# Kernel optimization log

Hardware: AMD Instinct MI355X
Metric: run time of the kernel (lower is better)

## Reference

```python
import jax, jax.numpy as jnp
import numpy as np

BS, SEQ, DIN, HID, H = 2, 2048, 1024, 1024, 16
D = HID // H  # head_size = 64

def setup_inputs() -> dict:
    key = jax.random.key(0)
    ks = jax.random.split(key, 9)
    s = 0.02
    return {
        "x":    jax.random.normal(ks[0], (BS, SEQ, DIN), jnp.float32),
        "Wq":   jax.random.normal(ks[1], (DIN, HID), jnp.float32) * s,
        "bq":   jax.random.normal(ks[2], (HID,), jnp.float32) * s,
        "Wk":   jax.random.normal(ks[3], (DIN, HID), jnp.float32) * s,
        "bk":   jax.random.normal(ks[4], (HID,), jnp.float32) * s,
        "Wv":   jax.random.normal(ks[5], (DIN, HID), jnp.float32) * s,
        "bv":   jax.random.normal(ks[6], (HID,), jnp.float32) * s,
        "Wmix": jax.random.normal(ks[7], (HID, HID), jnp.float32) * s,
        "bmix": jax.random.normal(ks[8], (HID,), jnp.float32) * s,
    }

def reference(x, Wq, bq, Wk, bk, Wv, bv, Wmix, bmix):
    bs, seq, _ = x.shape
    scale = jnp.asarray(D ** 0.5, x.dtype)
    # projections, split heads: [b, s, H, D] (contiguous channel slices per head,
    # equivalent to the torch transpose/reshape dance)
    q = (x @ Wq + bq).reshape(bs, seq, H, D)
    k = (x @ Wk + bk).reshape(bs, seq, H, D)
    v = (x @ Wv + bv).reshape(bs, seq, H, D)
    scores = jnp.einsum('bqhd,bkhd->bhqk', q, k) / scale  # [b, H, seq, seq]
    causal_mask = jnp.triu(jnp.ones((seq, seq), bool), k=1)
    scores = jnp.where(causal_mask, -jnp.inf, scores)
    probs = jax.nn.softmax(scores, axis=-1)
    att = jnp.einsum('bhqk,bkhd->bqhd', probs, v).reshape(bs, seq, HID)
    return att @ Wmix + bmix
```

## Files before the change

### kernel.cpp

```cpp
#include <hip/hip_runtime.h>
#include <hip/hip_bf16.h>

#define BS 2
#define SEQ 2048
#define DIN 1024
#define HID 1024
#define NH 16
#define HD 64
#define M_ROWS (BS*SEQ)
#define NQKV 3072

typedef __attribute__((ext_vector_type(8))) short short8;
typedef __attribute__((ext_vector_type(4))) short short4v;
typedef __attribute__((ext_vector_type(8))) __bf16 bf16x8;
typedef __attribute__((ext_vector_type(4))) float floatx4;

__device__ __forceinline__ short f2bf(float f) {
  return __builtin_bit_cast(short, (__bf16)f);
}
__device__ __forceinline__ float bf2f(short s) {
  return __uint_as_float(((unsigned)(unsigned short)s) << 16);
}

__device__ __forceinline__ floatx4 mfma16(short8 a, short8 b, floatx4 c) {
  return __builtin_amdgcn_mfma_f32_16x16x32_bf16(
      __builtin_bit_cast(bf16x8, a), __builtin_bit_cast(bf16x8, b), c, 0, 0, 0);
}

__device__ __forceinline__ float exp2fast(float x) {
#if __has_builtin(__builtin_amdgcn_exp2f)
  return __builtin_amdgcn_exp2f(x);
#else
  return exp2f(x);
#endif
}

__device__ __forceinline__ void gload_lds16(const void* g, void* l) {
  __builtin_amdgcn_global_load_lds(
      (const __attribute__((address_space(1))) unsigned int*)g,
      (__attribute__((address_space(3))) unsigned int*)l, 16, 0, 0);
}

__device__ __forceinline__ void lds_w8s(short* base, int row, int colsh, short8 v) {
  *(short8*)((char*)base + row * 128 + ((colsh * 2) ^ ((row & 7) << 4))) = v;
}
__device__ __forceinline__ void lds_w4s(short* base, int row, int colsh, short4v v) {
  *(short4v*)((char*)base + row * 128 + ((colsh * 2) ^ ((row & 7) << 4))) = v;
}
__device__ __forceinline__ short8 lds_r8s(const short* base, int row, int colsh) {
  return *(const short8*)((const char*)base + row * 128 + ((colsh * 2) ^ ((row & 7) << 4)));
}

__global__ __launch_bounds__(256) void convx_kernel(const float* __restrict__ x,
                                                    short* __restrict__ xb) {
  int gid = blockIdx.x * 256 + threadIdx.x;
  const float4* x4 = (const float4*)x;
  float4 v0 = x4[2 * gid], v1 = x4[2 * gid + 1];
  short8 o;
  o[0] = f2bf(v0.x); o[1] = f2bf(v0.y); o[2] = f2bf(v0.z); o[3] = f2bf(v0.w);
  o[4] = f2bf(v1.x); o[5] = f2bf(v1.y); o[6] = f2bf(v1.z); o[7] = f2bf(v1.w);
  *(short8*)&xb[(size_t)gid * 8] = o;
}

__global__ __launch_bounds__(256) void transw_kernel(
    const float* __restrict__ Wq, const float* __restrict__ Wk,
    const float* __restrict__ Wv, const float* __restrict__ Wmix,
    short* __restrict__ Wt, short* __restrict__ Wmixt)
{
  __shared__ float Ws[64][65];
  const float* src; short* dst;
  switch (blockIdx.z) {
    case 0:  src = Wq;   dst = Wt;                 break;
    case 1:  src = Wk;   dst = Wt + (1u << 20);    break;
    case 2:  src = Wv;   dst = Wt + (2u << 20);    break;
    default: src = Wmix; dst = Wmixt;              break;
  }
  const int n0 = blockIdx.x * 64, k0 = blockIdx.y * 64;
  const int c = threadIdx.x & 63, r0 = threadIdx.x >> 6;
  #pragma unroll
  for (int i = 0; i < 16; ++i) {
    int rr = r0 + 4 * i;
    Ws[rr][c] = src[(size_t)(k0 + rr) * DIN + n0 + c];
  }
  __syncthreads();
  #pragma unroll
  for (int i = 0; i < 16; ++i) {
    int cc = r0 + 4 * i;
    dst[(size_t)(n0 + cc) * DIN + k0 + c] = f2bf(Ws[c][cc]);
  }
}

template<int BM, int BN, bool OUT_F32, bool QKV>
__global__ __launch_bounds__(256) void gemm_kernel(
    const short* __restrict__ A, const short* __restrict__ Bt,
    const float* __restrict__ bias0, const float* __restrict__ bias1,
    const float* __restrict__ bias2, void* __restrict__ Cp,
    short* __restrict__ vt, int Ndim, int Kdim)
{
  constexpr int MT = BM / 32, NT = BN / 32;
  __shared__ short As[BM * 64];
  __shared__ short Bs[BN * 64];
  const int tid = threadIdx.x;
  const int wid = tid >> 6, lane = tid & 63, lg = lane >> 4, lm = lane & 15;
  const int wr = wid >> 1, wc = wid & 1;
  const int m0 = blockIdx.y * BM, n0 = blockIdx.x * BN;

  floatx4 acc[MT][NT];
  #pragma unroll
  for (int i = 0; i < MT; ++i)
    #pragma unroll
    for (int j = 0; j < NT; ++j) acc[i][j] = floatx4{0.f, 0.f, 0.f, 0.f};

  for (int k0 = 0; k0 < Kdim; k0 += 64) {
    __syncthreads();
    #pragma unroll
    for (int j = 0; j < BM / 32; ++j) {
      int flat = tid + 256 * j;
      int row = flat >> 3, ch = (flat & 7) ^ (row & 7);
      gload_lds16(A + (size_t)(m0 + row) * Kdim + k0 + ch * 8,
                  (char*)As + wid * 1024 + j * 4096);
    }
    #pragma unroll
    for (int j = 0; j < BN / 32; ++j) {
      int flat = tid + 256 * j;
      int row = flat >> 3, ch = (flat & 7) ^ (row & 7);
      gload_lds16(Bt + (size_t)(n0 + row) * Kdim + k0 + ch * 8,
                  (char*)Bs + wid * 1024 + j * 4096);
    }
    __syncthreads();

    #pragma unroll
    for (int kk = 0; kk < 2; ++kk) {
      short8 a[MT], b[NT];
      #pragma unroll
      for (int mt = 0; mt < MT; ++mt) {
        int row = wr * (BM / 2) + mt * 16 + lm;
        int ch = (kk * 4 + lg) ^ (row & 7);
        a[mt] = *(const short8*)&As[row * 64 + ch * 8];
      }
      #pragma unroll
      for (int nt = 0; nt < NT; ++nt) {
        int row = wc * (BN / 2) + nt * 16 + lm;
        int ch = (kk * 4 + lg) ^ (row & 7);
        b[nt] = *(const short8*)&Bs[row * 64 + ch * 8];
      }
      #pragma unroll
      for (int mt = 0; mt < MT; ++mt)
        #pragma unroll
        for (int nt = 0; nt < NT; ++nt)
          acc[mt][nt] = mfma16(a[mt], b[nt], acc[mt][nt]);
    }
  }

  #pragma unroll
  for (int mt = 0; mt < MT; ++mt) {
    const int row0 = m0 + wr * (BM / 2) + mt * 16 + 4 * lg;
    #pragma unroll
    for (int nt = 0; nt < NT; ++nt) {
      const int col = n0 + wc * (BN / 2) + nt * 16 + lm;
      const float* bp = bias0;
      if (QKV) bp = (col < 1024) ? bias0 : (col < 2048 ? bias1 : bias2);
      const float bv = bp[col & 1023];
      if (QKV && n0 >= 2048) {
        int hd = col - 2048;
        int bb = row0 >> 11, s = row0 & 2047;
        short4v pv;
        #pragma unroll
        for (int r = 0; r < 4; ++r) pv[r] = f2bf(acc[mt][nt][r] + bv);
        *(short4v*)&vt[((size_t)(bb * (NH * HD) + hd)) * SEQ + s] = pv;
      } else {
        #pragma unroll
        for (int r = 0; r < 4; ++r) {
          float v = acc[mt][nt][r] + bv;
          if (OUT_F32) ((float*)Cp)[(size_t)(row0 + r) * Ndim + col] = v;
          else         ((short*)Cp)[(size_t)(row0 + r) * Ndim + col] = f2bf(v);
        }
      }
    }
  }
}

#define MFIX 12.0f
__global__ __launch_bounds__(256) void attn_kernel(
    const short* __restrict__ qkv, const short* __restrict__ vt,
    short* __restrict__ att, short* __restrict__ pO, float* __restrict__ pml)
{
  __shared__ short Ks[2 * 64 * 64];
  __shared__ short Vs[2 * 64 * 64];
  __shared__ short Ps[4 * 16 * 64];
  const int tid = threadIdx.x;
  const int wid = tid >> 6, lane = tid & 63, lg = lane >> 4, lm = lane & 15;

  int id = blockIdx.x, x, c;
  if (id < 4)        { x = id;                       c = 0;        }
  else if (id < 12)  { int t = id - 4;   x = 4  + (t >> 1); c = t & 1; }
  else if (id < 24)  { int t = id - 12;  x = 8  + t / 3;    c = t % 3; }
  else if (id < 40)  { int t = id - 24;  x = 12 + (t >> 2); c = t & 3; }
  else if (id < 60)  { int t = id - 40;  x = 16 + t / 5;    c = t % 5; }
  else if (id < 84)  { int t = id - 60;  x = 20 + t / 6;    c = t % 6; }
  else if (id < 112) { int t = id - 84;  x = 24 + t / 7;    c = t % 7; }
  else               { int t = id - 112; x = 28 + (t >> 3); c = t & 7; }
  const int nch = (x >> 2) + 1;
  const int tb = c * 4;
  const int te = min(tb + 4, x + 1);
  const int q0 = x * 64;
  const int bh = blockIdx.y, b = bh >> 4, h = bh & 15;
  const short* qp = qkv + (size_t)(b * SEQ) * NQKV + h * HD;
  const short* kp = qp + HID;
  const short* vp = vt + (size_t)bh * HD * SEQ;

  const float cl2 = 0.18033688011112042f;
  const int qrow_g = q0 + wid * 16 + lm;
  short8 qf[2];
  {
    const short* qrow = qp + (size_t)qrow_g * NQKV;
    #pragma unroll
    for (int kk = 0; kk < 2; ++kk) {
      short8 raw = *(const short8*)(qrow + kk * 32 + lg * 8);
      #pragma unroll
      for (int j = 0; j < 8; ++j) qf[kk][j] = f2bf(bf2f(raw[j]) * cl2);
    }
  }

  short8 ones;
  #pragma unroll
  for (int j = 0; j < 8; ++j) ones[j] = (short)0x3F80;

  const int rstage = tid >> 3, c8 = (tid & 7) * 8;
  short8 kreg[2], vreg[2];
  #pragma unroll
  for (int i = 0; i < 2; ++i) {
    kreg[i] = *(const short8*)(kp + (size_t)(tb * 64 + rstage + 32 * i) * NQKV + c8);
    vreg[i] = *(const short8*)(vp + (size_t)(rstage + 32 * i) * SEQ + tb * 64 + c8);
  }

  short* psw = Ps + wid * 16 * 64;
  floatx4 o[4];
  floatx4 ol = floatx4{0.f, 0.f, 0.f, 0.f};
  #pragma unroll
  for (int nt = 0; nt < 4; ++nt) o[nt] = floatx4{0.f, 0.f, 0.f, 0.f};

  for (int t = tb; t < te; ++t) {
    const int cb = (t - tb) & 1;
    short* Kb = Ks + cb * (64 * 64);
    short* Vb = Vs + cb * (64 * 64);
    #pragma unroll
    for (int i = 0; i < 2; ++i) {
      lds_w8s(Kb, rstage + 32 * i, c8, kreg[i]);
      lds_w8s(Vb, rstage + 32 * i, c8, vreg[i]);
    }
    if (t + 1 < te) {
      const int kv1 = (t + 1) * 64;
      #pragma unroll
      for (int i = 0; i < 2; ++i) {
        kreg[i] = *(const short8*)(kp + (size_t)(kv1 + rstage + 32 * i) * NQKV + c8);
        vreg[i] = *(const short8*)(vp + (size_t)(rstage + 32 * i) * SEQ + kv1 + c8);
      }
    }
    __syncthreads();

    floatx4 s[4];
    #pragma unroll
    for (int nt = 0; nt < 4; ++nt) s[nt] = floatx4{-MFIX, -MFIX, -MFIX, -MFIX};
    __builtin_amdgcn_s_setprio(1);
    #pragma unroll
    for (int kk = 0; kk < 2; ++kk)
      #pragma unroll
      for (int nt = 0; nt < 4; ++nt)
        s[nt] = mfma16(lds_r8s(Kb, nt * 16 + lm, kk * 32 + lg * 8), qf[kk], s[nt]);
    __builtin_amdgcn_s_setprio(0);

    if (t == x) {
      #pragma unroll
      for (int nt = 0; nt < 4; ++nt)
        #pragma unroll
        for (int r = 0; r < 4; ++r) {
          int kv = t * 64 + nt * 16 + 4 * lg + r;
          if (kv > qrow_g) s[nt][r] = -3e38f;
        }
    }

    #pragma unroll
    for (int nt = 0; nt < 4; ++nt) {
      short4v pv;
      #pragma unroll
      for (int r = 0; r < 4; ++r) pv[r] = f2bf(exp2fast(s[nt][r]));
      lds_w4s(psw, lm, nt * 16 + 4 * lg, pv);
    }

    #pragma unroll
    for (int kk = 0; kk < 2; ++kk) {
      short8 pf = lds_r8s(psw, lm, kk * 32 + lg * 8);
      __builtin_amdgcn_s_setprio(1);
      #pragma unroll
      for (int nt = 0; nt < 4; ++nt)
        o[nt] = mfma16(lds_r8s(Vb, nt * 16 + lm, kk * 32 + lg * 8), pf, o[nt]);
      ol = mfma16(ones, pf, ol);
      __builtin_amdgcn_s_setprio(0);
    }
  }

  if (nch == 1) {
    const float linv = 1.0f / ol[0];
    #pragma unroll
    for (int nt = 0; nt < 4; ++nt) {
      short4v ov;
      #pragma unroll
      for (int r = 0; r < 4; ++r) ov[r] = f2bf(o[nt][r] * linv);
      *(short4v*)&att[((size_t)(b * SEQ + qrow_g)) * HID + h * HD + nt * 16 + 4 * lg] = ov;
    }
  } else {
    const int g = x >> 2;
    const int slot = bh * 140 + (2 * g * g + 2 * g - 4 + (x & 3) * (g + 1)) + c;
    short* po = pO + (size_t)slot * 4096;
    const int ql = wid * 16 + lm;
    #pragma unroll
    for (int nt = 0; nt < 4; ++nt) {
      short4v ov;
      #pragma unroll
      for (int r = 0; r < 4; ++r) ov[r] = f2bf(o[nt][r]);
      *(short4v*)&po[ql * 64 + nt * 16 + 4 * lg] = ov;
    }
    if (lane < 16) {
      pml[slot * 128 + 64 + ql] = ol[0];
    }
  }
}

__global__ __launch_bounds__(256) void combine_kernel(
    const short* __restrict__ pO, const float* __restrict__ pml,
    short* __restrict__ att)
{
  const int x = 4 + blockIdx.x;
  const int bh = blockIdx.y, b = bh >> 4, h = bh & 15;
  const int g = x >> 2;
  const int nch = g + 1;
  const int tid = threadIdx.x;
  const int row = tid >> 2, d0 = (tid & 3) * 16;
  const int base_slot = bh * 140 + (2 * g * g + 2 * g - 4 + (x & 3) * (g + 1));

  float L = 0.f;
  for (int cc = 0; cc < nch; ++cc)
    L += pml[(base_slot + cc) * 128 + 64 + row];
  const float inv = 1.0f / L;

  float acc[16];
  #pragma unroll
  for (int j = 0; j < 16; ++j) acc[j] = 0.f;
  for (int cc = 0; cc < nch; ++cc) {
    const short* po = pO + (size_t)(base_slot + cc) * 4096 + row * 64 + d0;
    short8 v0 = *(const short8*)po, v1 = *(const short8*)(po + 8);
    #pragma unroll
    for (int j = 0; j < 8; ++j) {
      acc[j]     += bf2f(v0[j]);
      acc[j + 8] += bf2f(v1[j]);
    }
  }
  short8 o0, o1;
  #pragma unroll
  for (int j = 0; j < 8; ++j) {
    o0[j] = f2bf(acc[j] * inv);
    o1[j] = f2bf(acc[j + 8] * inv);
  }
  short* dst = att + ((size_t)(b * SEQ + x * 64 + row)) * HID + h * HD + d0;
  *(short8*)dst = o0;
  *(short8*)(dst + 8) = o1;
}

extern "C" void kernel_launch(void* const* d_in, const int* in_sizes, int n_in,
                              void* d_out, int out_size, void* d_ws, size_t ws_size,
                              hipStream_t stream) {
  (void)in_sizes; (void)n_in; (void)out_size; (void)ws_size;
  const float* x    = (const float*)d_in[0];
  const float* Wq   = (const float*)d_in[1];
  const float* bq   = (const float*)d_in[2];
  const float* Wk   = (const float*)d_in[3];
  const float* bk   = (const float*)d_in[4];
  const float* Wv   = (const float*)d_in[5];
  const float* bv   = (const float*)d_in[6];
  const float* Wmix = (const float*)d_in[7];
  const float* bmix = (const float*)d_in[8];
  float* out = (float*)d_out;

  char* w = (char*)d_ws;
  short* xb      = (short*)w; w += (size_t)8 << 20;
  short* Wt      = (short*)w; w += (size_t)6 << 20;
  short* Wmixt   = (short*)w; w += (size_t)2 << 20;
  short* qkvb    = (short*)w; w += (size_t)24 << 20;
  short* vtb     = (short*)w; w += (size_t)8 << 20;
  short* ab      = (short*)w; w += (size_t)8 << 20;
  short* pO      = (short*)w; w += (size_t)140 * 32 * 4096 * 2;
  float* pml     = (float*)w;

  hipLaunchKernelGGL(convx_kernel, dim3(2048), dim3(256), 0, stream, x, xb);
  hipLaunchKernelGGL(transw_kernel, dim3(16, 16, 4), dim3(256), 0, stream,
                     Wq, Wk, Wv, Wmix, Wt, Wmixt);

  hipLaunchKernelGGL((gemm_kernel<128, 128, false, true>), dim3(NQKV / 128, M_ROWS / 128),
                     dim3(256), 0, stream, xb, Wt, bq, bk, bv, (void*)qkvb, vtb, NQKV, DIN);

  hipLaunchKernelGGL(attn_kernel, dim3(144, BS * NH), dim3(256), 0, stream,
                     qkvb, vtb, ab, pO, pml);
  hipLaunchKernelGGL(combine_kernel, dim3(28, BS * NH), dim3(256), 0, stream,
                     pO, pml, ab);

  hipLaunchKernelGGL((gemm_kernel<64, 128, true, false>), dim3(HID / 128, M_ROWS / 64),
                     dim3(256), 0, stream, ab, Wmixt, bmix, bmix, bmix, (void*)out,
                     (short*)nullptr, HID, DIN);
}
```

Before: 109.9 us.

## Merge x conversion and weight transpose kernels; precompute attention LDS offsets

Folds the x fp32-to-bf16 conversion into the weight transpose kernel as an extra z-slice, which removes one kernel launch. In the attention kernel, swizzled LDS offsets are precomputed once outside the loop and global K/V pointers are advanced incrementally, cutting per-iteration integer address arithmetic. It also adds a launch-bounds occupancy hint of 4 to the attention kernel, which may limit registers.

Measured after the change: 105.7 us. 1.04x faster.

```diff
diff --git a/kernel.cpp b/kernel.cpp
--- a/kernel.cpp
+++ b/kernel.cpp
@@ -41,52 +41,51 @@
       (__attribute__((address_space(3))) unsigned int*)l, 16, 0, 0);
 }
 
-__device__ __forceinline__ void lds_w8s(short* base, int row, int colsh, short8 v) {
-  *(short8*)((char*)base + row * 128 + ((colsh * 2) ^ ((row & 7) << 4))) = v;
-}
-__device__ __forceinline__ void lds_w4s(short* base, int row, int colsh, short4v v) {
-  *(short4v*)((char*)base + row * 128 + ((colsh * 2) ^ ((row & 7) << 4))) = v;
-}
-__device__ __forceinline__ short8 lds_r8s(const short* base, int row, int colsh) {
-  return *(const short8*)((const char*)base + row * 128 + ((colsh * 2) ^ ((row & 7) << 4)));
-}
-
-__global__ __launch_bounds__(256) void convx_kernel(const float* __restrict__ x,
-                                                    short* __restrict__ xb) {
-  int gid = blockIdx.x * 256 + threadIdx.x;
-  const float4* x4 = (const float4*)x;
-  float4 v0 = x4[2 * gid], v1 = x4[2 * gid + 1];
-  short8 o;
-  o[0] = f2bf(v0.x); o[1] = f2bf(v0.y); o[2] = f2bf(v0.z); o[3] = f2bf(v0.w);
-  o[4] = f2bf(v1.x); o[5] = f2bf(v1.y); o[6] = f2bf(v1.z); o[7] = f2bf(v1.w);
-  *(short8*)&xb[(size_t)gid * 8] = o;
-}
-
-__global__ __launch_bounds__(256) void transw_kernel(
+__device__ __forceinline__ int swz_off(int row, int colsh) {
+  return row * 128 + ((colsh * 2) ^ ((row & 7) << 4));
+}
+
+__global__ __launch_bounds__(256) void prep_kernel(
+    const float* __restrict__ x,
     const float* __restrict__ Wq, const float* __restrict__ Wk,
     const float* __restrict__ Wv, const float* __restrict__ Wmix,
-    short* __restrict__ Wt, short* __restrict__ Wmixt)
+    short* __restrict__ xb, short* __restrict__ Wt, short* __restrict__ Wmixt)
 {
   __shared__ float Ws[64][65];
-  const float* src; short* dst;
-  switch (blockIdx.z) {
-    case 0:  src = Wq;   dst = Wt;                 break;
-    case 1:  src = Wk;   dst = Wt + (1u << 20);    break;
-    case 2:  src = Wv;   dst = Wt + (2u << 20);    break;
-    default: src = Wmix; dst = Wmixt;              break;
-  }
-  const int n0 = blockIdx.x * 64, k0 = blockIdx.y * 64;
-  const int c = threadIdx.x & 63, r0 = threadIdx.x >> 6;
-  #pragma unroll
-  for (int i = 0; i < 16; ++i) {
-    int rr = r0 + 4 * i;
-    Ws[rr][c] = src[(size_t)(k0 + rr) * DIN + n0 + c];
-  }
-  __syncthreads();
-  #pragma unroll
-  for (int i = 0; i < 16; ++i) {
-    int cc = r0 + 4 * i;
-    dst[(size_t)(n0 + cc) * DIN + k0 + c] = f2bf(Ws[c][cc]);
+  if (blockIdx.z < 4) {
+    const float* src; short* dst;
+    switch (blockIdx.z) {
+      case 0:  src = Wq;   dst = Wt;                 break;
+      case 1:  src = Wk;   dst = Wt + (1u << 20);    break;
+      case 2:  src = Wv;   dst = Wt + (2u << 20);    break;
+      default: src = Wmix; dst = Wmixt;              break;
+    }
+    const int n0 = blockIdx.x * 64, k0 = blockIdx.y * 64;
+    const int c = threadIdx.x & 63, r0 = threadIdx.x >> 6;
+    #pragma unroll
+    for (int i = 0; i < 16; ++i) {
+      int rr = r0 + 4 * i;
+      Ws[rr][c] = src[(size_t)(k0 + rr) * DIN + n0 + c];
+    }
+    __syncthreads();
+    #pragma unroll
+    for (int i = 0; i < 16; ++i) {
+      int cc = r0 + 4 * i;
+      dst[(size_t)(n0 + cc) * DIN + k0 + c] = f2bf(Ws[c][cc]);
+    }
+  } else {
+    const int bb = blockIdx.y * 16 + blockIdx.x;
+    const int gid0 = bb * 256 + threadIdx.x;
+    const float4* x4 = (const float4*)x;
+    #pragma unroll
+    for (int it = 0; it < 8; ++it) {
+      int gid = gid0 + it * 65536;
+      float4 v0 = x4[2 * gid], v1 = x4[2 * gid + 1];
+      short8 o;
+      o[0] = f2bf(v0.x); o[1] = f2bf(v0.y); o[2] = f2bf(v0.z); o[3] = f2bf(v0.w);
+      o[4] = f2bf(v1.x); o[5] = f2bf(v1.y); o[6] = f2bf(v1.z); o[7] = f2bf(v1.w);
+      *(short8*)&xb[(size_t)gid * 8] = o;
+    }
   }
 }
 
@@ -181,7 +180,7 @@
 }
 
 #define MFIX 12.0f
-__global__ __launch_bounds__(256) void attn_kernel(
+__global__ __launch_bounds__(256, 4) void attn_kernel(
     const short* __restrict__ qkv, const short* __restrict__ vt,
     short* __restrict__ att, short* __restrict__ pO, float* __restrict__ pml)
 {
@@ -227,14 +226,31 @@
   for (int j = 0; j < 8; ++j) ones[j] = (short)0x3F80;
 
   const int rstage = tid >> 3, c8 = (tid & 7) * 8;
+  int soff[2], koff[2][4], pw[4], pr[2];
+  #pragma unroll
+  for (int i = 0; i < 2; ++i) soff[i] = swz_off(rstage + 32 * i, c8);
+  #pragma unroll
+  for (int kk = 0; kk < 2; ++kk)
+    #pragma unroll
+    for (int nt = 0; nt < 4; ++nt)
+      koff[kk][nt] = swz_off(nt * 16 + lm, kk * 32 + lg * 8);
+  #pragma unroll
+  for (int nt = 0; nt < 4; ++nt) pw[nt] = swz_off(lm, nt * 16 + 4 * lg);
+  #pragma unroll
+  for (int kk = 0; kk < 2; ++kk) pr[kk] = swz_off(lm, kk * 32 + lg * 8);
+
+  const short* kgp[2];
+  const short* vgp[2];
   short8 kreg[2], vreg[2];
   #pragma unroll
   for (int i = 0; i < 2; ++i) {
-    kreg[i] = *(const short8*)(kp + (size_t)(tb * 64 + rstage + 32 * i) * NQKV + c8);
-    vreg[i] = *(const short8*)(vp + (size_t)(rstage + 32 * i) * SEQ + tb * 64 + c8);
-  }
-
-  short* psw = Ps + wid * 16 * 64;
+    kgp[i] = kp + (size_t)(tb * 64 + rstage + 32 * i) * NQKV + c8;
+    vgp[i] = vp + (size_t)(rstage + 32 * i) * SEQ + tb * 64 + c8;
+    kreg[i] = *(const short8*)kgp[i];
+    vreg[i] = *(const short8*)vgp[i];
+  }
+
+  char* psw = (char*)(Ps + wid * 16 * 64);
   floatx4 o[4];
   floatx4 ol = floatx4{0.f, 0.f, 0.f, 0.f};
   #pragma unroll
@@ -242,19 +258,20 @@
 
   for (int t = tb; t < te; ++t) {
     const int cb = (t - tb) & 1;
-    short* Kb = Ks + cb * (64 * 64);
-    short* Vb = Vs + cb * (64 * 64);
+    char* Kb = (char*)Ks + cb * 8192;
+    char* Vb = (char*)Vs + cb * 8192;
     #pragma unroll
     for (int i = 0; i < 2; ++i) {
-      lds_w8s(Kb, rstage + 32 * i, c8, kreg[i]);
-      lds_w8s(Vb, rstage + 32 * i, c8, vreg[i]);
+      *(short8*)(Kb + soff[i]) = kreg[i];
+      *(short8*)(Vb + soff[i]) = vreg[i];
     }
     if (t + 1 < te) {
-      const int kv1 = (t + 1) * 64;
       #pragma unroll
       for (int i = 0; i < 2; ++i) {
-        kreg[i] = *(const short8*)(kp + (size_t)(kv1 + rstage + 32 * i) * NQKV + c8);
-        vreg[i] = *(const short8*)(vp + (size_t)(rstage + 32 * i) * SEQ + kv1 + c8);
+        kgp[i] += 64 * NQKV;
+        vgp[i] += 64;
+        kreg[i] = *(const short8*)kgp[i];
+        vreg[i] = *(const short8*)vgp[i];
       }
     }
     __syncthreads();
@@ -267,7 +284,7 @@
     for (int kk = 0; kk < 2; ++kk)
       #pragma unroll
       for (int nt = 0; nt < 4; ++nt)
-        s[nt] = mfma16(lds_r8s(Kb, nt * 16 + lm, kk * 32 + lg * 8), qf[kk], s[nt]);
+        s[nt] = mfma16(*(const short8*)(Kb + koff[kk][nt]), qf[kk], s[nt]);
     __builtin_amdgcn_s_setprio(0);
 
     if (t == x) {
@@ -285,16 +302,16 @@
       short4v pv;
       #pragma unroll
       for (int r = 0; r < 4; ++r) pv[r] = f2bf(exp2fast(s[nt][r]));
-      lds_w4s(psw, lm, nt * 16 + 4 * lg, pv);
+      *(short4v*)(psw + pw[nt]) = pv;
     }
 
     #pragma unroll
     for (int kk = 0; kk < 2; ++kk) {
-      short8 pf = lds_r8s(psw, lm, kk * 32 + lg * 8);
+      short8 pf = *(const short8*)(psw + pr[kk]);
       __builtin_amdgcn_s_setprio(1);
       #pragma unroll
       for (int nt = 0; nt < 4; ++nt)
-        o[nt] = mfma16(lds_r8s(Vb, nt * 16 + lm, kk * 32 + lg * 8), pf, o[nt]);
+        o[nt] = mfma16(*(const short8*)(Vb + koff[kk][nt]), pf, o[nt]);
       ol = mfma16(ones, pf, ol);
       __builtin_amdgcn_s_setprio(0);
     }
@@ -392,9 +409,8 @@
   short* pO      = (short*)w; w += (size_t)140 * 32 * 4096 * 2;
   float* pml     = (float*)w;
 
-  hipLaunchKernelGGL(convx_kernel, dim3(2048), dim3(256), 0, stream, x, xb);
-  hipLaunchKernelGGL(transw_kernel, dim3(16, 16, 4), dim3(256), 0, stream,
-                     Wq, Wk, Wv, Wmix, Wt, Wmixt);
+  hipLaunchKernelGGL(prep_kernel, dim3(16, 16, 5), dim3(256), 0, stream,
+                     x, Wq, Wk, Wv, Wmix, xb, Wt, Wmixt);
 
   hipLaunchKernelGGL((gemm_kernel<128, 128, false, true>), dim3(NQKV / 128, M_ROWS / 128),
                      dim3(256), 0, stream, xb, Wt, bq, bk, bv, (void*)qkvb, vtb, NQKV, DIN);
```
